# Kernel tuning notes

Measured on AMD Instinct MI355X. Metric: run time of the kernel, lower is better.

The kernel has to match this reference:

```python
import jax, jax.numpy as jnp
import numpy as np

N_NODES = 50000
HIDDEN = 64
N_EDGES = 1200000


def setup_inputs() -> dict:
    key = jax.random.key(0)
    ks = jax.random.split(key, 12)
    x = jax.random.normal(ks[0], (N_NODES, HIDDEN), dtype=jnp.float32)
    edge_index = jax.random.randint(ks[1], (2, N_EDGES), 0, N_NODES, dtype=jnp.int64)
    s = 1.0 / np.sqrt(HIDDEN)
    # RGCN layer (single relation): relation weight, root weight, bias
    W_rel1 = jax.random.normal(ks[2], (HIDDEN, HIDDEN), dtype=jnp.float32) * s
    W_root1 = jax.random.normal(ks[3], (HIDDEN, HIDDEN), dtype=jnp.float32) * s
    b1 = jnp.zeros((HIDDEN,), dtype=jnp.float32)
    # Three GraphConv layers: self weight, neighbor weight, bias each
    W_self2 = jax.random.normal(ks[4], (HIDDEN, HIDDEN), dtype=jnp.float32) * s
    W_nbr2 = jax.random.normal(ks[5], (HIDDEN, HIDDEN), dtype=jnp.float32) * s
    b2 = jnp.zeros((HIDDEN,), dtype=jnp.float32)
    W_self3 = jax.random.normal(ks[6], (HIDDEN, HIDDEN), dtype=jnp.float32) * s
    W_nbr3 = jax.random.normal(ks[7], (HIDDEN, HIDDEN), dtype=jnp.float32) * s
    b3 = jnp.zeros((HIDDEN,), dtype=jnp.float32)
    W_self4 = jax.random.normal(ks[8], (HIDDEN, HIDDEN), dtype=jnp.float32) * s
    W_nbr4 = jax.random.normal(ks[9], (HIDDEN, HIDDEN), dtype=jnp.float32) * s
    b4 = jnp.zeros((HIDDEN,), dtype=jnp.float32)
    return {
        "x": x, "edge_index": edge_index,
        "W_rel1": W_rel1, "W_root1": W_root1, "b1": b1,
        "W_self2": W_self2, "W_nbr2": W_nbr2, "b2": b2,
        "W_self3": W_self3, "W_nbr3": W_nbr3, "b3": b3,
        "W_self4": W_self4, "W_nbr4": W_nbr4, "b4": b4,
    }


def _rgcn(x, W_rel, W_root, b, src, dst, n_nodes):
    # single-relation RGCN: root transform + mean-aggregated relation transform
    msg = x[src] @ W_rel                                   # [E, H]
    agg = jax.ops.segment_sum(msg, dst, num_segments=n_nodes)
    cnt = jax.ops.segment_sum(jnp.ones((src.shape[0],), x.dtype), dst, num_segments=n_nodes)
    agg = agg / jnp.maximum(cnt, 1.0)[:, None]
    return x @ W_root + agg + b


def _graphconv(x, W_self, W_nbr, b, src, dst, n_nodes):
    # GraphConv: self transform + sum-aggregated neighbor transform
    agg = jax.ops.segment_sum(x[src], dst, num_segments=n_nodes)  # [N, H]
    return x @ W_self + agg @ W_nbr + b


def reference(x, edge_index, W_rel1, W_root1, b1, W_self2, W_nbr2, b2,
              W_self3, W_nbr3, b3, W_self4, W_nbr4, b4):
    n = x.shape[0]
    src, dst = edge_index[0], edge_index[1]
    h = jax.nn.relu(_rgcn(x, W_rel1, W_root1, b1, src, dst, n))
    h = jax.nn.relu(_graphconv(h, W_self2, W_nbr2, b2, src, dst, n))
    x_1 = h
    h = jax.nn.relu(_graphconv(h, W_self3, W_nbr3, b3, src, dst, n))
    h = jax.nn.relu(_graphconv(h, W_self4, W_nbr4, b4, src, dst, n))
    x_2 = h
    return (x_1, x_2)
```

## Files before the change

kernel.cpp:

```cpp
#include <hip/hip_runtime.h>
#include <hip/hip_fp16.h>

#define N_NODES 50000
#define HIDDEN  64
#define N_EDGES 1200000

#define BSHIFT 7
#define BUKSZ  128
#define NBUK   391
#define GBIN   512
#define PAD2   6144
#define FWAVES 12500
#define FBLK   (FWAVES / 4)
#define NPW    4

typedef unsigned short ushort_t;
typedef _Float16 hf2 __attribute__((ext_vector_type(2)));

__device__ __forceinline__ float bcastf(float v, int k) {
    return __int_as_float(__builtin_amdgcn_readlane(__float_as_int(v), k));
}
__device__ __forceinline__ hf2 u2h(unsigned u) { union { unsigned u; hf2 h; } x; x.u = u; return x.h; }
__device__ __forceinline__ unsigned h2u(hf2 h) { union { hf2 h; unsigned u; } x; x.h = h; return x.u; }
__device__ __forceinline__ unsigned pkh(float a, float b) {
    __half2 h = __float22half2_rn(make_float2(a, b));
    union { __half2 h; unsigned u; } x; x.h = h; return x.u;
}
__device__ __forceinline__ ushort_t f2h(float a) {
    __half h = __float2half_rn(a);
    union { __half h; ushort_t u; } x; x.h = h; return x.u;
}
__device__ __forceinline__ void bfly(float4& a) {
    a.x += __shfl_xor(a.x, 16); a.y += __shfl_xor(a.y, 16);
    a.z += __shfl_xor(a.z, 16); a.w += __shfl_xor(a.w, 16);
    a.x += __shfl_xor(a.x, 32); a.y += __shfl_xor(a.y, 32);
    a.z += __shfl_xor(a.z, 32); a.w += __shfl_xor(a.w, 32);
}

__global__ __launch_bounds__(512) void init_kernel(int* __restrict__ cursor,
                                                   const float* __restrict__ Wn2, const float* __restrict__ Ws2,
                                                   const float* __restrict__ Wn3, const float* __restrict__ Ws3,
                                                   const float* __restrict__ Wn4, const float* __restrict__ Ws4,
                                                   uint4* __restrict__ pw) {
    int b = blockIdx.x, tid = threadIdx.x;
    if (b == 0) {
        if (tid < NBUK) cursor[tid] = tid * PAD2;
    } else {
        int layer = b - 1;
        const float* Wn = (layer == 0) ? Wn2 : (layer == 1) ? Wn3 : Wn4;
        const float* Ws = (layer == 0) ? Ws2 : (layer == 1) ? Ws3 : Ws4;
        int kp = tid >> 4, q = tid & 15;
        {
            const float4 a = *(const float4*)(Wn + (2 * kp) * 64 + 4 * q);
            const float4 c = *(const float4*)(Wn + (2 * kp + 1) * 64 + 4 * q);
            pw[layer * 1024 + tid] = make_uint4(pkh(a.x, c.x), pkh(a.y, c.y), pkh(a.z, c.z), pkh(a.w, c.w));
        }
        {
            const float4 a = *(const float4*)(Ws + (2 * kp) * 64 + 4 * q);
            const float4 c = *(const float4*)(Ws + (2 * kp + 1) * 64 + 4 * q);
            pw[layer * 1024 + 512 + tid] = make_uint4(pkh(a.x, c.x), pkh(a.y, c.y), pkh(a.z, c.z), pkh(a.w, c.w));
        }
    }
}

__global__ __launch_bounds__(256) void scatter_fused_kernel(const int* __restrict__ ei,
                                                            int* __restrict__ cursor,
                                                            int* __restrict__ tmp, int E) {
    __shared__ int h[NBUK];
    __shared__ int cur[NBUK];
    int tid = threadIdx.x;
    for (int b = tid; b < NBUK; b += 256) h[b] = 0;
    __syncthreads();
    for (int e = blockIdx.x * 256 + tid; e < E; e += GBIN * 256)
        atomicAdd(&h[ei[E + e] >> BSHIFT], 1);
    __syncthreads();
    for (int b = tid; b < NBUK; b += 256) cur[b] = atomicAdd(&cursor[b], h[b]);
    __syncthreads();
    for (int e = blockIdx.x * 256 + tid; e < E; e += GBIN * 256) {
        int src = ei[e];
        int dst = ei[E + e];
        int p = atomicAdd(&cur[dst >> BSHIFT], 1);
        tmp[p] = src | ((dst & (BUKSZ - 1)) << 16);
    }
}

__global__ __launch_bounds__(512) void bucketize_kernel(const int* __restrict__ tmp,
                                                        const int* __restrict__ cursor,
                                                        int2* __restrict__ row_info,
                                                        ushort_t* __restrict__ csr,
                                                        const float* __restrict__ x,
                                                        const float* __restrict__ Wrel,
                                                        const float* __restrict__ Wroot,
                                                        const float* __restrict__ bias,
                                                        ushort_t* __restrict__ tbf,
                                                        ushort_t* __restrict__ ubf) {
    __shared__ int hist[BUKSZ];
    __shared__ int cur[BUKSZ];
    __shared__ ushort_t stage[PAD2];
    int b = blockIdx.x, tid = threadIdx.x;
    if (b < NBUK) {
        int base = b * PAD2;
        int count = cursor[b] - base;
        int node_base = b << BSHIFT;
        if (tid < BUKSZ) hist[tid] = 0;
        __syncthreads();
        for (int i = tid; i < count; i += 512)
            atomicAdd(&hist[tmp[base + i] >> 16], 1);
        __syncthreads();
        int v = (tid < BUKSZ) ? hist[tid] : 0;
        int vr = (v + 15) & ~15;
        __syncthreads();
        if (tid < BUKSZ) hist[tid] = vr;
#pragma unroll
        for (int o = 1; o < BUKSZ; o <<= 1) {
            __syncthreads();
            int y = (tid >= o && tid < BUKSZ) ? hist[tid - o] : 0;
            __syncthreads();
            if (tid < BUKSZ) hist[tid] += y;
        }
        __syncthreads();
        int excl = 0;
        if (tid < BUKSZ) {
            excl = hist[tid] - vr;
            cur[tid] = excl;
            int node = node_base + tid;
            if (node < N_NODES) row_info[node] = make_int2(base + excl, v);
        }
        __syncthreads();
        if (tid < BUKSZ) {
            for (int p = v; p < vr; ++p) stage[excl + p] = (ushort_t)N_NODES;
        }
        for (int i = tid; i < count; i += 512) {
            int p = tmp[base + i];
            int slot = atomicAdd(&cur[p >> 16], 1);
            stage[slot] = (ushort_t)(p & 0xFFFF);
        }
        __syncthreads();
        int total = hist[BUKSZ - 1];
        for (int i = tid; i < total; i += 512)
            csr[base + i] = stage[i];
    } else {
        int lane = tid & 63;
        float wn[64], ws[64];
#pragma unroll
        for (int k = 0; k < 64; ++k) {
            wn[k] = Wrel[k * 64 + lane];
            ws[k] = Wroot[k * 64 + lane];
        }
        float bv = bias[lane];
        int wave = (b - NBUK) * 8 + (tid >> 6);
        int nwaves = (gridDim.x - NBUK) * 8;
        if (wave == 0) tbf[(size_t)N_NODES * 64 + lane] = 0;
        for (int i = wave; i < N_NODES; i += nwaves) {
            float hv = x[i * 64 + lane];
            float tacc = 0.f, uacc = bv;
#pragma unroll
            for (int k = 0; k < 64; ++k) {
                float hk = bcastf(hv, k);
                tacc = fmaf(hk, wn[k], tacc);
                uacc = fmaf(hk, ws[k], uacc);
            }
            tbf[(size_t)i * 64 + lane] = f2h(tacc);
            ubf[(size_t)i * 64 + lane] = f2h(uacc);
        }
    }
}

__device__ __forceinline__ uint2 ldrow(const ushort_t* __restrict__ tbf, int s, int q) {
    return *(const uint2*)(tbf + (size_t)s * 64 + q * 4);
}

__device__ __forceinline__ float4 agg_core_p(const ushort_t* __restrict__ tbf,
                                             const ushort_t* __restrict__ csr,
                                             int start, int deg, int g, int q, uint2 iv) {
    const ushort_t* cp = csr + start;
    hf2 l0{0,0}, l1{0,0}, l2{0,0}, l3{0,0};
    hf2 m0{0,0}, m1{0,0}, m2{0,0}, m3{0,0};
    int vr = (deg + 15) & ~15;
    for (int base = 0; base < vr; base += 16) {
        int s0 = (int)(iv.x & 0xFFFF);
        int s1 = (int)(iv.x >> 16);
        int s2 = (int)(iv.y & 0xFFFF);
        int s3 = (int)(iv.y >> 16);
        const uint2 w0 = ldrow(tbf, s0, q);
        const uint2 w1 = ldrow(tbf, s1, q);
        const uint2 w2 = ldrow(tbf, s2, q);
        const uint2 w3 = ldrow(tbf, s3, q);
        int nb = base + 16;
        iv = *(const uint2*)(cp + ((nb < vr) ? nb + 4 * g : 4 * g));
        l0 += u2h(w0.x); m0 += u2h(w0.y);
        l1 += u2h(w1.x); m1 += u2h(w1.y);
        l2 += u2h(w2.x); m2 += u2h(w2.y);
        l3 += u2h(w3.x); m3 += u2h(w3.y);
    }
    hf2 lo = (l0 + l1) + (l2 + l3);
    hf2 hi = (m0 + m1) + (m2 + m3);
    float4 acc = make_float4((float)lo.x, (float)lo.y, (float)hi.x, (float)hi.y);
    bfly(acc);
    return acc;
}

__device__ __forceinline__ float4 unpack_u2(uint2 uv) {
    hf2 a = u2h(uv.x), b = u2h(uv.y);
    return make_float4((float)a.x, (float)a.y, (float)b.x, (float)b.y);
}

__global__ __launch_bounds__(256, 6) void fused_kernel(const ushort_t* __restrict__ tin,
                                                       const ushort_t* __restrict__ uin,
                                                       const int2* __restrict__ row_info,
                                                       const ushort_t* __restrict__ csr,
                                                       const uint4* __restrict__ pwL,
                                                       const float* __restrict__ bias_next,
                                                       ushort_t* __restrict__ tout,
                                                       ushort_t* __restrict__ uout,
                                                       float* __restrict__ dout,
                                                       int use_mean) {
    __shared__ uint4 wlds[1024];
    __shared__ float blds[64];
    int tid = threadIdx.x;
    for (int i = tid; i < 1024; i += 256) wlds[i] = pwL[i];
    if (tid < 64) blds[tid] = bias_next[tid];
    if (blockIdx.x == 0 && tid < 32)
        ((unsigned*)(tout + (size_t)N_NODES * 64))[tid] = 0;
    __syncthreads();
    int lane = tid & 63, g = lane >> 4, q = lane & 15;
    int w = blockIdx.x * 4 + (tid >> 6);

    int2 ri[NPW];
    uint2 iv0[NPW];
    uint2 uvp[NPW];
#pragma unroll
    for (int i = 0; i < NPW; ++i) ri[i] = row_info[w + FWAVES * i];
#pragma unroll
    for (int i = 0; i < NPW; ++i) iv0[i] = *(const uint2*)(csr + ri[i].x + 4 * g);
#pragma unroll
    for (int i = 0; i < NPW; ++i)
        uvp[i] = *(const uint2*)(uin + (size_t)(w + FWAVES * i) * 64 + q * 4);

#pragma unroll
    for (int i = 0; i < NPW; ++i) {
        int node = w + FWAVES * i;
        float4 acc = agg_core_p(tin, csr, ri[i].x, ri[i].y, g, q, iv0[i]);
        float sc = use_mean ? 1.f / fmaxf((float)ri[i].y, 1.f) : 1.f;
        const float4 uv = unpack_u2(uvp[i]);
        float4 h;
        h.x = fmaxf(uv.x + acc.x * sc, 0.f);
        h.y = fmaxf(uv.y + acc.y * sc, 0.f);
        h.z = fmaxf(uv.z + acc.z * sc, 0.f);
        h.w = fmaxf(uv.w + acc.w * sc, 0.f);
        if (dout && g == 0)
            *(float4*)(dout + (size_t)node * 64 + q * 4) = h;
        int hp_lo = (int)pkh(h.x, h.y);
        int hp_hi = (int)pkh(h.z, h.w);
        float4 tp{0,0,0,0}, up{0,0,0,0};
#pragma unroll
        for (int jp = 0; jp < 8; ++jp) {
            int kp = 8 * g + jp;
            const uint4 wvn = wlds[kp * 16 + q];
            const uint4 wvs = wlds[512 + kp * 16 + q];
            int srcl = 4 * g + (jp >> 1);
            unsigned hu = (unsigned)__shfl((jp & 1) ? hp_hi : hp_lo, srcl);
            hf2 hh = u2h(hu);
            tp.x = __builtin_amdgcn_fdot2(hh, u2h(wvn.x), tp.x, false);
            tp.y = __builtin_amdgcn_fdot2(hh, u2h(wvn.y), tp.y, false);
            tp.z = __builtin_amdgcn_fdot2(hh, u2h(wvn.z), tp.z, false);
            tp.w = __builtin_amdgcn_fdot2(hh, u2h(wvn.w), tp.w, false);
            up.x = __builtin_amdgcn_fdot2(hh, u2h(wvs.x), up.x, false);
            up.y = __builtin_amdgcn_fdot2(hh, u2h(wvs.y), up.y, false);
            up.z = __builtin_amdgcn_fdot2(hh, u2h(wvs.z), up.z, false);
            up.w = __builtin_amdgcn_fdot2(hh, u2h(wvs.w), up.w, false);
        }
        bfly(tp); bfly(up);
        if (g == 0) {
            const float4 bv = *(const float4*)&blds[q * 4];
            uint2 upk, tpk;
            upk.x = pkh(up.x + bv.x, up.y + bv.y);
            upk.y = pkh(up.z + bv.z, up.w + bv.w);
            tpk.x = pkh(tp.x, tp.y);
            tpk.y = pkh(tp.z, tp.w);
            *(uint2*)(uout + (size_t)node * 64 + q * 4) = upk;
            *(uint2*)(tout + (size_t)node * 64 + q * 4) = tpk;
        }
    }
}

__global__ __launch_bounds__(256, 8) void agg_kernel(const ushort_t* __restrict__ tbf,
                                                     const ushort_t* __restrict__ ubf,
                                                     const int2* __restrict__ row_info,
                                                     const ushort_t* __restrict__ csr,
                                                     float* __restrict__ out, int use_mean) {
    int lane = threadIdx.x & 63;
    int g = lane >> 4, q = lane & 15;
    int node = (blockIdx.x * 256 + threadIdx.x) >> 6;
    if (node >= N_NODES) return;
    int2 ri = row_info[node];
    uint2 iv0 = *(const uint2*)(csr + ri.x + 4 * g);
    float4 acc = agg_core_p(tbf, csr, ri.x, ri.y, g, q, iv0);
    float scale = use_mean ? 1.f / fmaxf((float)ri.y, 1.f) : 1.f;
    if (g == 0) {
        const uint2 uvr = *(const uint2*)(ubf + (size_t)node * 64 + q * 4);
        const float4 uv = unpack_u2(uvr);
        float4 r;
        r.x = fmaxf(uv.x + acc.x * scale, 0.f);
        r.y = fmaxf(uv.y + acc.y * scale, 0.f);
        r.z = fmaxf(uv.z + acc.z * scale, 0.f);
        r.w = fmaxf(uv.w + acc.w * scale, 0.f);
        *(float4*)(out + (size_t)node * 64 + q * 4) = r;
    }
}

extern "C" void kernel_launch(void* const* d_in, const int* in_sizes, int n_in,
                              void* d_out, int out_size, void* d_ws, size_t ws_size,
                              hipStream_t stream) {
    const float* x      = (const float*)d_in[0];
    const int*   ei     = (const int*)d_in[1];
    const float* Wrel1  = (const float*)d_in[2];
    const float* Wroot1 = (const float*)d_in[3];
    const float* b1     = (const float*)d_in[4];
    const float* Wself2 = (const float*)d_in[5];
    const float* Wnbr2  = (const float*)d_in[6];
    const float* b2     = (const float*)d_in[7];
    const float* Wself3 = (const float*)d_in[8];
    const float* Wnbr3  = (const float*)d_in[9];
    const float* b3     = (const float*)d_in[10];
    const float* Wself4 = (const float*)d_in[11];
    const float* Wnbr4  = (const float*)d_in[12];
    const float* b4     = (const float*)d_in[13];

    const int N = N_NODES, E = N_EDGES;

    auto align = [](size_t o) { return (o + 255) & ~(size_t)255; };
    char* base = (char*)d_ws;
    size_t off = 0;
    int*  cursor   = (int*)(base + off);  off = align(off + (size_t)NBUK * 4);
    int2* row_info = (int2*)(base + off); off = align(off + (size_t)N * 8);
    int*  tmp      = (int*)(base + off);  off = align(off + (size_t)NBUK * PAD2 * 4);
    ushort_t* csr  = (ushort_t*)(base + off); off = align(off + (size_t)NBUK * PAD2 * 2 + 1024);
    uint4* pw      = (uint4*)(base + off);    off = align(off + (size_t)3 * 1024 * 16);
    ushort_t* tbA  = (ushort_t*)(base + off); off = align(off + (size_t)(N + 1) * 64 * 2);
    ushort_t* tbB  = (ushort_t*)(base + off); off = align(off + (size_t)(N + 1) * 64 * 2);
    ushort_t* ubA  = (ushort_t*)(base + off); off = align(off + (size_t)N * 64 * 2);
    ushort_t* ubB  = (ushort_t*)(base + off); off = align(off + (size_t)N * 64 * 2);

    float* out1 = (float*)d_out;
    float* out2 = (float*)d_out + (size_t)N * 64;

    init_kernel<<<4, 512, 0, stream>>>(cursor, Wnbr2, Wself2, Wnbr3, Wself3, Wnbr4, Wself4, pw);
    scatter_fused_kernel<<<GBIN, 256, 0, stream>>>(ei, cursor, tmp, E);
    bucketize_kernel<<<NBUK + 1024, 512, 0, stream>>>(tmp, cursor, row_info, csr,
                                                      x, Wrel1, Wroot1, b1, tbA, ubA);
    fused_kernel<<<FBLK, 256, 0, stream>>>(tbA, ubA, row_info, csr, pw,        b2, tbB, ubB, nullptr, 1);
    fused_kernel<<<FBLK, 256, 0, stream>>>(tbB, ubB, row_info, csr, pw + 1024, b3, tbA, ubA, out1, 0);
    fused_kernel<<<FBLK, 256, 0, stream>>>(tbA, ubA, row_info, csr, pw + 2048, b4, tbB, ubB, nullptr, 0);
    agg_kernel<<<(N + 3) / 4, 256, 0, stream>>>(tbB, ubB, row_info, csr, out2, 0);
}
```

Before: 276.7 us.

## Gather neighbor rows with 16-byte loads across 8 lanes, reduce in fp16

```diff
diff --git a/kernel.cpp b/kernel.cpp
--- a/kernel.cpp
+++ b/kernel.cpp
@@ -35,6 +35,9 @@
     a.z += __shfl_xor(a.z, 16); a.w += __shfl_xor(a.w, 16);
     a.x += __shfl_xor(a.x, 32); a.y += __shfl_xor(a.y, 32);
     a.z += __shfl_xor(a.z, 32); a.w += __shfl_xor(a.w, 32);
+}
+__device__ __forceinline__ hf2 sxor(hf2 v, int m) {
+    return v + u2h((unsigned)__shfl_xor((int)h2u(v), m));
 }
 
 __global__ __launch_bounds__(512) void init_kernel(int* __restrict__ cursor,
@@ -166,43 +169,31 @@
     }
 }
 
-__device__ __forceinline__ uint2 ldrow(const ushort_t* __restrict__ tbf, int s, int q) {
-    return *(const uint2*)(tbf + (size_t)s * 64 + q * 4);
-}
-
-__device__ __forceinline__ float4 agg_core_p(const ushort_t* __restrict__ tbf,
-                                             const ushort_t* __restrict__ csr,
-                                             int start, int deg, int g, int q, uint2 iv) {
+__device__ __forceinline__ void agg8(const ushort_t* __restrict__ tbf,
+                                     const ushort_t* __restrict__ csr,
+                                     int start, int deg, int e, int c,
+                                     unsigned iv0, float f[8]) {
     const ushort_t* cp = csr + start;
-    hf2 l0{0,0}, l1{0,0}, l2{0,0}, l3{0,0};
-    hf2 m0{0,0}, m1{0,0}, m2{0,0}, m3{0,0};
+    hf2 a0{0,0}, a1{0,0}, a2{0,0}, a3{0,0};
+    hf2 b0{0,0}, b1{0,0}, b2{0,0}, b3{0,0};
     int vr = (deg + 15) & ~15;
+    unsigned iv = iv0;
     for (int base = 0; base < vr; base += 16) {
-        int s0 = (int)(iv.x & 0xFFFF);
-        int s1 = (int)(iv.x >> 16);
-        int s2 = (int)(iv.y & 0xFFFF);
-        int s3 = (int)(iv.y >> 16);
-        const uint2 w0 = ldrow(tbf, s0, q);
-        const uint2 w1 = ldrow(tbf, s1, q);
-        const uint2 w2 = ldrow(tbf, s2, q);
-        const uint2 w3 = ldrow(tbf, s3, q);
+        int sA = (int)(iv & 0xFFFF);
+        int sB = (int)(iv >> 16);
+        const uint4 wA = *(const uint4*)(tbf + (size_t)sA * 64 + c * 8);
+        const uint4 wB = *(const uint4*)(tbf + (size_t)sB * 64 + c * 8);
         int nb = base + 16;
-        iv = *(const uint2*)(cp + ((nb < vr) ? nb + 4 * g : 4 * g));
-        l0 += u2h(w0.x); m0 += u2h(w0.y);
-        l1 += u2h(w1.x); m1 += u2h(w1.y);
-        l2 += u2h(w2.x); m2 += u2h(w2.y);
-        l3 += u2h(w3.x); m3 += u2h(w3.y);
-    }
-    hf2 lo = (l0 + l1) + (l2 + l3);
-    hf2 hi = (m0 + m1) + (m2 + m3);
-    float4 acc = make_float4((float)lo.x, (float)lo.y, (float)hi.x, (float)hi.y);
-    bfly(acc);
-    return acc;
-}
-
-__device__ __forceinline__ float4 unpack_u2(uint2 uv) {
-    hf2 a = u2h(uv.x), b = u2h(uv.y);
-    return make_float4((float)a.x, (float)a.y, (float)b.x, (float)b.y);
+        iv = *(const unsigned*)(cp + ((nb < vr) ? nb : 0) + 2 * e);
+        a0 += u2h(wA.x); a1 += u2h(wA.y); a2 += u2h(wA.z); a3 += u2h(wA.w);
+        b0 += u2h(wB.x); b1 += u2h(wB.y); b2 += u2h(wB.z); b3 += u2h(wB.w);
+    }
+    hf2 s0 = a0 + b0, s1 = a1 + b1, s2 = a2 + b2, s3 = a3 + b3;
+    s0 = sxor(s0, 8);  s1 = sxor(s1, 8);  s2 = sxor(s2, 8);  s3 = sxor(s3, 8);
+    s0 = sxor(s0, 16); s1 = sxor(s1, 16); s2 = sxor(s2, 16); s3 = sxor(s3, 16);
+    s0 = sxor(s0, 32); s1 = sxor(s1, 32); s2 = sxor(s2, 32); s3 = sxor(s3, 32);
+    f[0] = (float)s0.x; f[1] = (float)s0.y; f[2] = (float)s1.x; f[3] = (float)s1.y;
+    f[4] = (float)s2.x; f[5] = (float)s2.y; f[6] = (float)s3.x; f[7] = (float)s3.y;
 }
 
 __global__ __launch_bounds__(256, 6) void fused_kernel(const ushort_t* __restrict__ tin,
@@ -223,43 +214,51 @@
     if (blockIdx.x == 0 && tid < 32)
         ((unsigned*)(tout + (size_t)N_NODES * 64))[tid] = 0;
     __syncthreads();
-    int lane = tid & 63, g = lane >> 4, q = lane & 15;
+    int lane = tid & 63;
+    int g = lane >> 4, q = lane & 15;
+    int e = lane >> 3, c = lane & 7;
     int w = blockIdx.x * 4 + (tid >> 6);
 
     int2 ri[NPW];
-    uint2 iv0[NPW];
-    uint2 uvp[NPW];
+    unsigned iv0[NPW];
+    uint4 uvp[NPW];
 #pragma unroll
     for (int i = 0; i < NPW; ++i) ri[i] = row_info[w + FWAVES * i];
 #pragma unroll
-    for (int i = 0; i < NPW; ++i) iv0[i] = *(const uint2*)(csr + ri[i].x + 4 * g);
+    for (int i = 0; i < NPW; ++i) iv0[i] = *(const unsigned*)(csr + ri[i].x + 2 * e);
 #pragma unroll
     for (int i = 0; i < NPW; ++i)
-        uvp[i] = *(const uint2*)(uin + (size_t)(w + FWAVES * i) * 64 + q * 4);
+        uvp[i] = *(const uint4*)(uin + (size_t)(w + FWAVES * i) * 64 + c * 8);
 
 #pragma unroll
     for (int i = 0; i < NPW; ++i) {
         int node = w + FWAVES * i;
-        float4 acc = agg_core_p(tin, csr, ri[i].x, ri[i].y, g, q, iv0[i]);
+        float f[8];
+        agg8(tin, csr, ri[i].x, ri[i].y, e, c, iv0[i], f);
         float sc = use_mean ? 1.f / fmaxf((float)ri[i].y, 1.f) : 1.f;
-        const float4 uv = unpack_u2(uvp[i]);
-        float4 h;
-        h.x = fmaxf(uv.x + acc.x * sc, 0.f);
-        h.y = fmaxf(uv.y + acc.y * sc, 0.f);
-        h.z = fmaxf(uv.z + acc.z * sc, 0.f);
-        h.w = fmaxf(uv.w + acc.w * sc, 0.f);
-        if (dout && g == 0)
-            *(float4*)(dout + (size_t)node * 64 + q * 4) = h;
-        int hp_lo = (int)pkh(h.x, h.y);
-        int hp_hi = (int)pkh(h.z, h.w);
+        hf2 ua = u2h(uvp[i].x), ub = u2h(uvp[i].y), uc = u2h(uvp[i].z), ud = u2h(uvp[i].w);
+        float h0 = fmaxf((float)ua.x + f[0] * sc, 0.f);
+        float h1 = fmaxf((float)ua.y + f[1] * sc, 0.f);
+        float h2 = fmaxf((float)ub.x + f[2] * sc, 0.f);
+        float h3 = fmaxf((float)ub.y + f[3] * sc, 0.f);
+        float h4 = fmaxf((float)uc.x + f[4] * sc, 0.f);
+        float h5 = fmaxf((float)uc.y + f[5] * sc, 0.f);
+        float h6 = fmaxf((float)ud.x + f[6] * sc, 0.f);
+        float h7 = fmaxf((float)ud.y + f[7] * sc, 0.f);
+        if (dout && lane < 8) {
+            *(float4*)(dout + (size_t)node * 64 + c * 8)     = make_float4(h0, h1, h2, h3);
+            *(float4*)(dout + (size_t)node * 64 + c * 8 + 4) = make_float4(h4, h5, h6, h7);
+        }
+        unsigned hp0 = pkh(h0, h1), hp1 = pkh(h2, h3), hp2 = pkh(h4, h5), hp3 = pkh(h6, h7);
         float4 tp{0,0,0,0}, up{0,0,0,0};
 #pragma unroll
         for (int jp = 0; jp < 8; ++jp) {
             int kp = 8 * g + jp;
             const uint4 wvn = wlds[kp * 16 + q];
             const uint4 wvs = wlds[512 + kp * 16 + q];
-            int srcl = 4 * g + (jp >> 1);
-            unsigned hu = (unsigned)__shfl((jp & 1) ? hp_hi : hp_lo, srcl);
+            int srcl = 2 * g + (jp >> 2);
+            unsigned hsel = (jp & 3) == 0 ? hp0 : (jp & 3) == 1 ? hp1 : (jp & 3) == 2 ? hp2 : hp3;
+            unsigned hu = (unsigned)__shfl((int)hsel, srcl);
             hf2 hh = u2h(hu);
             tp.x = __builtin_amdgcn_fdot2(hh, u2h(wvn.x), tp.x, false);
             tp.y = __builtin_amdgcn_fdot2(hh, u2h(wvn.y), tp.y, false);
@@ -290,22 +289,28 @@
                                                      const ushort_t* __restrict__ csr,
                                                      float* __restrict__ out, int use_mean) {
     int lane = threadIdx.x & 63;
-    int g = lane >> 4, q = lane & 15;
+    int e = lane >> 3, c = lane & 7;
     int node = (blockIdx.x * 256 + threadIdx.x) >> 6;
     if (node >= N_NODES) return;
     int2 ri = row_info[node];
-    uint2 iv0 = *(const uint2*)(csr + ri.x + 4 * g);
-    float4 acc = agg_core_p(tbf, csr, ri.x, ri.y, g, q, iv0);
-    float scale = use_mean ? 1.f / fmaxf((float)ri.y, 1.f) : 1.f;
-    if (g == 0) {
-        const uint2 uvr = *(const uint2*)(ubf + (size_t)node * 64 + q * 4);
-        const float4 uv = unpack_u2(uvr);
-        float4 r;
-        r.x = fmaxf(uv.x + acc.x * scale, 0.f);
-        r.y = fmaxf(uv.y + acc.y * scale, 0.f);
-        r.z = fmaxf(uv.z + acc.z * scale, 0.f);
-        r.w = fmaxf(uv.w + acc.w * scale, 0.f);
-        *(float4*)(out + (size_t)node * 64 + q * 4) = r;
+    unsigned iv0 = *(const unsigned*)(csr + ri.x + 2 * e);
+    uint4 uv4 = *(const uint4*)(ubf + (size_t)node * 64 + c * 8);
+    float f[8];
+    agg8(tbf, csr, ri.x, ri.y, e, c, iv0, f);
+    float sc = use_mean ? 1.f / fmaxf((float)ri.y, 1.f) : 1.f;
+    if (lane < 8) {
+        hf2 ua = u2h(uv4.x), ub = u2h(uv4.y), uc = u2h(uv4.z), ud = u2h(uv4.w);
+        float4 r0, r1;
+        r0.x = fmaxf((float)ua.x + f[0] * sc, 0.f);
+        r0.y = fmaxf((float)ua.y + f[1] * sc, 0.f);
+        r0.z = fmaxf((float)ub.x + f[2] * sc, 0.f);
+        r0.w = fmaxf((float)ub.y + f[3] * sc, 0.f);
+        r1.x = fmaxf((float)uc.x + f[4] * sc, 0.f);
+        r1.y = fmaxf((float)uc.y + f[5] * sc, 0.f);
+        r1.z = fmaxf((float)ud.x + f[6] * sc, 0.f);
+        r1.w = fmaxf((float)ud.y + f[7] * sc, 0.f);
+        *(float4*)(out + (size_t)node * 64 + c * 8)     = r0;
+        *(float4*)(out + (size_t)node * 64 + c * 8 + 4) = r1;
     }
 }
 
```

After: 577.2 us. +108.6%, slower.
